# Optimization experiments

Measured on AMD Instinct MI355X. Metric: run time of the kernel, lower is better.

The kernel has to match this reference:

```python
import jax, jax.numpy as jnp
import numpy as np

N_NODES = 100000
N_EDGES = 1600000
D_FEAT = 32
K = 5


def _spmm(edge_row, edge_col, edge_vals, feat):
    # y[i] = sum_{e: row[e]==i} vals[e] * feat[col[e]]  -- sparse A @ feat
    msgs = edge_vals[:, None] * feat[edge_col]  # [E, d]
    return jax.ops.segment_sum(msgs, edge_row, num_segments=N_NODES)


def setup_inputs() -> dict:
    key = jax.random.key(0)
    k1, k2, k3, k4, k5 = jax.random.split(key, 5)
    feat = jax.random.normal(k1, (N_NODES, D_FEAT), dtype=jnp.float32)
    # approximate D^{-1/2} A D^{-1/2} magnitudes: ~1/avg_degree so spectrum stays bounded
    edge_vals = jax.random.uniform(k2, (N_EDGES,), dtype=jnp.float32) * (1.0 / 16.0)
    theta = jnp.asarray([0.5, 0.4, 0.3, 0.2, 0.1], dtype=jnp.float32)
    edge_row = jax.random.randint(k3, (N_EDGES,), 0, N_NODES, dtype=jnp.int32)
    edge_col = jax.random.randint(k4, (N_EDGES,), 0, N_NODES, dtype=jnp.int32)
    return {"feat": feat, "edge_vals": edge_vals, "theta": theta,
            "edge_row": edge_row, "edge_col": edge_col}


def reference(feat, edge_vals, theta, edge_row, edge_col):
    # h = theta[0]*feat; for k>=1: feat = feat - A@feat; h += theta[k]*feat
    h = theta[0] * feat
    for k in range(1, K):
        feat = feat - _spmm(edge_row, edge_col, edge_vals, feat)
        h = h + theta[k] * feat
    return h
```

## Files before the change

kernel.cpp:

```cpp
#include <hip/hip_runtime.h>

#define N_NODES 100000
#define N_EDGES 1600000
#define D_FEAT 32
#define KPOLY 5

#define NWIN 512
#define RPW  ((N_NODES + NWIN - 1) / NWIN)
#define WPAD 16
#define CAP  4096

#define VAL_SCALE 524288.0f
#define VAL_INV   (1.0f / 524288.0f)

#define EB_BS  256
#define EB_EPT 16
#define EB_EPB (EB_BS * EB_EPT)
#define EB_NB  ((N_EDGES + EB_EPB - 1) / EB_EPB)

__device__ __forceinline__ unsigned short f2bf(float f) {
    unsigned u = __float_as_uint(f);
    unsigned r = u + 0x7fffu + ((u >> 16) & 1u);
    return (unsigned short)(r >> 16);
}
__device__ __forceinline__ float bfl(unsigned u) { return __uint_as_float(u << 16); }
__device__ __forceinline__ float bfh(unsigned u) { return __uint_as_float(u & 0xffff0000u); }


__global__ void init_and_bf16_kernel(int* __restrict__ win_cursor,
                                     const float* __restrict__ feat,
                                     unsigned short* __restrict__ out, int n4) {
    int i = blockIdx.x * blockDim.x + threadIdx.x;
    if (i < NWIN) win_cursor[i * WPAD] = i * CAP;
    if (i >= n4) return;
    float4 f = reinterpret_cast<const float4*>(feat)[i];
    ushort4 o;
    o.x = f2bf(f.x); o.y = f2bf(f.y); o.z = f2bf(f.z); o.w = f2bf(f.w);
    reinterpret_cast<ushort4*>(out)[i] = o;
}


__global__ __launch_bounds__(EB_BS) void bucket_kernel(const int* __restrict__ row,
                                                       const int* __restrict__ col,
                                                       const float* __restrict__ vals,
                                                       int* __restrict__ win_cursor,
                                                       uint2* __restrict__ pile) {
    __shared__ int wcnt[NWIN];
    __shared__ int wbase[NWIN];
    int t = threadIdx.x;
    for (int i = t; i < NWIN; i += EB_BS) wcnt[i] = 0;
    __syncthreads();
    int base = blockIdx.x * EB_EPB;
    int w_[EB_EPT];
    int r_[EB_EPT];
#pragma unroll
    for (int i = 0; i < EB_EPT; ++i) {
        int e = base + i * EB_BS + t;
        if (e < N_EDGES) {
            int r = row[e];
            int w = r / RPW;
            r_[i] = r; w_[i] = w;
            atomicAdd(&wcnt[w], 1);
        } else w_[i] = -1;
    }
    __syncthreads();
    for (int i = t; i < NWIN; i += EB_BS) {
        wbase[i] = wcnt[i] ? atomicAdd(&win_cursor[i * WPAD], wcnt[i]) : 0;
        wcnt[i] = 0;
    }
    __syncthreads();
#pragma unroll
    for (int i = 0; i < EB_EPT; ++i) {
        int w = w_[i];
        if (w < 0) continue;
        int e = base + i * EB_BS + t;
        int loc = atomicAdd(&wcnt[w], 1);
        unsigned fx = (unsigned)__float2int_rn(vals[e] * VAL_SCALE);
        if (fx > 0x7FFFu) fx = 0x7FFFu;
        uint2 ed;
        ed.x = ((unsigned)col[e] << 15) | fx;
        ed.y = (unsigned)(r_[i] - w * RPW);
        pile[wbase[w] + loc] = ed;
    }
}

__global__ __launch_bounds__(256) void finesort_kernel(const uint2* __restrict__ pile,
                                                       const int* __restrict__ win_cursor,
                                                       unsigned int* __restrict__ cvout,
                                                       int2* __restrict__ row_rng) {
    __shared__ int cnt[256];
    __shared__ int incl[256];
    __shared__ int cur[256];
    int w = blockIdx.x, t = threadIdx.x;
    int rbeg = w * RPW;
    int rcnt = N_NODES - rbeg;
    if (rcnt > RPW) rcnt = RPW;
    if (rcnt < 0) rcnt = 0;
    int pbeg = w * CAP;
    int pend = win_cursor[w * WPAD];
    cnt[t] = 0;
    __syncthreads();
    for (int i = pbeg + t; i < pend; i += 256) atomicAdd(&cnt[pile[i].y], 1);
    __syncthreads();
    int v = cnt[t];
    incl[t] = v;
    __syncthreads();
    for (int off = 1; off < 256; off <<= 1) {
        int u = (t >= off) ? incl[t - off] : 0;
        __syncthreads();
        incl[t] += u;
        __syncthreads();
    }
    int ex = incl[t] - v;
    if (t < rcnt) {
        cur[t] = ex;
        row_rng[rbeg + t] = make_int2(pbeg + ex, pbeg + ex + v);
    }
    __syncthreads();
    for (int i = pbeg + t; i < pend; i += 256) {
        uint2 ed = pile[i];
        int pos = atomicAdd(&cur[ed.y], 1);
        cvout[pbeg + pos] = ed.x;
    }
}


__global__ __launch_bounds__(256) void spmm_kernel(const int2* __restrict__ row_rng,
                               const unsigned int* __restrict__ cv,
                               const unsigned short* __restrict__ gsrc,
                               const float* __restrict__ feat,
                               unsigned short* __restrict__ g_out,
                               float* __restrict__ h,
                               const float* __restrict__ theta,
                               int k, int first, int write_cur) {
    int tid = blockIdx.x * blockDim.x + threadIdx.x;
    int r = tid >> 2;
    int c = tid & 3;
    if (r >= N_NODES) return;
    float t = theta[k];
    int2 rng = row_rng[r];
    int e = rng.x, end = rng.y;
    float a0=0.f,a1=0.f,a2=0.f,a3=0.f,a4=0.f,a5=0.f,a6=0.f,a7=0.f;

    for (; e + 4 <= end; e += 4) {
        unsigned p0 = cv[e + 0];
        unsigned p1 = cv[e + 1];
        unsigned p2 = cv[e + 2];
        unsigned p3 = cv[e + 3];
        uint4 q0 = *(reinterpret_cast<const uint4*>(gsrc + (size_t)(p0 >> 15) * D_FEAT) + c);
        uint4 q1 = *(reinterpret_cast<const uint4*>(gsrc + (size_t)(p1 >> 15) * D_FEAT) + c);
        uint4 q2 = *(reinterpret_cast<const uint4*>(gsrc + (size_t)(p2 >> 15) * D_FEAT) + c);
        uint4 q3 = *(reinterpret_cast<const uint4*>(gsrc + (size_t)(p3 >> 15) * D_FEAT) + c);
        float v0 = (float)(p0 & 0x7FFFu) * VAL_INV;
        float v1 = (float)(p1 & 0x7FFFu) * VAL_INV;
        float v2 = (float)(p2 & 0x7FFFu) * VAL_INV;
        float v3 = (float)(p3 & 0x7FFFu) * VAL_INV;
        a0 += v0 * bfl(q0.x); a1 += v0 * bfh(q0.x); a2 += v0 * bfl(q0.y); a3 += v0 * bfh(q0.y);
        a4 += v0 * bfl(q0.z); a5 += v0 * bfh(q0.z); a6 += v0 * bfl(q0.w); a7 += v0 * bfh(q0.w);
        a0 += v1 * bfl(q1.x); a1 += v1 * bfh(q1.x); a2 += v1 * bfl(q1.y); a3 += v1 * bfh(q1.y);
        a4 += v1 * bfl(q1.z); a5 += v1 * bfh(q1.z); a6 += v1 * bfl(q1.w); a7 += v1 * bfh(q1.w);
        a0 += v2 * bfl(q2.x); a1 += v2 * bfh(q2.x); a2 += v2 * bfl(q2.y); a3 += v2 * bfh(q2.y);
        a4 += v2 * bfl(q2.z); a5 += v2 * bfh(q2.z); a6 += v2 * bfl(q2.w); a7 += v2 * bfh(q2.w);
        a0 += v3 * bfl(q3.x); a1 += v3 * bfh(q3.x); a2 += v3 * bfl(q3.y); a3 += v3 * bfh(q3.y);
        a4 += v3 * bfl(q3.z); a5 += v3 * bfh(q3.z); a6 += v3 * bfl(q3.w); a7 += v3 * bfh(q3.w);
    }
    for (; e < end; ++e) {
        unsigned p = cv[e];
        float v = (float)(p & 0x7FFFu) * VAL_INV;
        uint4 q = *(reinterpret_cast<const uint4*>(gsrc + (size_t)(p >> 15) * D_FEAT) + c);
        a0 += v * bfl(q.x); a1 += v * bfh(q.x); a2 += v * bfl(q.y); a3 += v * bfh(q.y);
        a4 += v * bfl(q.z); a5 += v * bfh(q.z); a6 += v * bfl(q.w); a7 += v * bfh(q.w);
    }

    size_t base = (size_t)r * D_FEAT + c * 8;
    float c0,c1,c2,c3,c4,c5,c6,c7;
    if (first) {
        float4 f0 = *reinterpret_cast<const float4*>(feat + base);
        float4 f1 = *reinterpret_cast<const float4*>(feat + base + 4);
        c0=f0.x; c1=f0.y; c2=f0.z; c3=f0.w; c4=f1.x; c5=f1.y; c6=f1.z; c7=f1.w;
    } else {
        uint4 q = *reinterpret_cast<const uint4*>(gsrc + base);
        c0=bfl(q.x); c1=bfh(q.x); c2=bfl(q.y); c3=bfh(q.y);
        c4=bfl(q.z); c5=bfh(q.z); c6=bfl(q.w); c7=bfh(q.w);
    }
    float n0=c0-a0, n1=c1-a1, n2=c2-a2, n3=c3-a3, n4=c4-a4, n5=c5-a5, n6=c6-a6, n7=c7-a7;
    if (write_cur) {
        uint4 o;
        o.x = (unsigned)f2bf(n0) | ((unsigned)f2bf(n1) << 16);
        o.y = (unsigned)f2bf(n2) | ((unsigned)f2bf(n3) << 16);
        o.z = (unsigned)f2bf(n4) | ((unsigned)f2bf(n5) << 16);
        o.w = (unsigned)f2bf(n6) | ((unsigned)f2bf(n7) << 16);
        *reinterpret_cast<uint4*>(g_out + base) = o;
    }
    float4 h0, h1;
    if (first) {
        float t0 = theta[0];
        h0.x = t0*c0; h0.y = t0*c1; h0.z = t0*c2; h0.w = t0*c3;
        h1.x = t0*c4; h1.y = t0*c5; h1.z = t0*c6; h1.w = t0*c7;
    } else {
        h0 = *reinterpret_cast<float4*>(h + base);
        h1 = *reinterpret_cast<float4*>(h + base + 4);
    }
    h0.x += t*n0; h0.y += t*n1; h0.z += t*n2; h0.w += t*n3;
    h1.x += t*n4; h1.y += t*n5; h1.z += t*n6; h1.w += t*n7;
    *reinterpret_cast<float4*>(h + base) = h0;
    *reinterpret_cast<float4*>(h + base + 4) = h1;
}

extern "C" void kernel_launch(void* const* d_in, const int* in_sizes, int n_in,
                              void* d_out, int out_size, void* d_ws, size_t ws_size,
                              hipStream_t stream) {
    const float* feat  = (const float*)d_in[0];
    const float* vals  = (const float*)d_in[1];
    const float* theta = (const float*)d_in[2];
    const int*   row   = (const int*)d_in[3];
    const int*   col   = (const int*)d_in[4];
    float* h = (float*)d_out;

    char* ws = (char*)d_ws;
    size_t off = 0;
    auto alloc = [&](size_t bytes) { void* p = ws + off; off = (off + bytes + 63) & ~(size_t)63; return p; };
    unsigned short* feat16 = (unsigned short*)alloc((size_t)N_NODES * D_FEAT * sizeof(short));
    unsigned short* T1 = (unsigned short*)alloc((size_t)N_NODES * D_FEAT * sizeof(short));
    unsigned short* T2 = (unsigned short*)alloc((size_t)N_NODES * D_FEAT * sizeof(short));
    unsigned short* T3 = (unsigned short*)alloc((size_t)N_NODES * D_FEAT * sizeof(short));
    int2*  row_rng  = (int2*)alloc((size_t)N_NODES * sizeof(int2));
    int*   win_cursor = (int*)alloc((size_t)NWIN * WPAD * sizeof(int));
    uint2* pile     = (uint2*)alloc((size_t)NWIN * CAP * sizeof(uint2));
    unsigned int* cv = (unsigned int*)alloc((size_t)NWIN * CAP * sizeof(unsigned int));

    const int blk = 256;
    const int n4 = N_NODES * D_FEAT / 4;

    init_and_bf16_kernel<<<(n4 + blk - 1) / blk, blk, 0, stream>>>(win_cursor, feat, feat16, n4);
    bucket_kernel<<<EB_NB, EB_BS, 0, stream>>>(row, col, vals, win_cursor, pile);
    finesort_kernel<<<NWIN, 256, 0, stream>>>(pile, win_cursor, cv, row_rng);

    const int sgrid = (N_NODES * 4 + blk - 1) / blk;
    spmm_kernel<<<sgrid, blk, 0, stream>>>(row_rng, cv, feat16, feat, T1, h, theta, 1, 1, 1);
    spmm_kernel<<<sgrid, blk, 0, stream>>>(row_rng, cv, T1, feat, T2, h, theta, 2, 0, 1);
    spmm_kernel<<<sgrid, blk, 0, stream>>>(row_rng, cv, T2, feat, T3, h, theta, 3, 0, 1);
    spmm_kernel<<<sgrid, blk, 0, stream>>>(row_rng, cv, T3, feat, T1, h, theta, 4, 0, 0);
}
```

Measured before the change: 151.8 us.

## Stage bucketed edges in shared memory for coalesced scatter to window piles

The bucket kernel now computes a block-local exclusive prefix sum of per-window counts and first writes packed edges into a shared-memory staging buffer sorted by window. A second pass then writes the staged edges to the global pile in contiguous runs per window, replacing scattered per-thread global stores. Edge packing also moves into the first pass so col and vals are read while row is loaded. This adds 32KB of LDS, extra syncs and a scan, which may lower occupancy.

```diff
diff --git a/kernel.cpp b/kernel.cpp
--- a/kernel.cpp
+++ b/kernel.cpp
@@ -46,41 +46,69 @@
                                                        int* __restrict__ win_cursor,
                                                        uint2* __restrict__ pile) {
     __shared__ int wcnt[NWIN];
+    __shared__ int lbase[NWIN];
     __shared__ int wbase[NWIN];
+    __shared__ int ps[EB_BS];
+    __shared__ uint2 stage[EB_EPB];
     int t = threadIdx.x;
     for (int i = t; i < NWIN; i += EB_BS) wcnt[i] = 0;
     __syncthreads();
+
     int base = blockIdx.x * EB_EPB;
-    int w_[EB_EPT];
-    int r_[EB_EPT];
+    unsigned pk_[EB_EPT];
+    int wr_[EB_EPT];
 #pragma unroll
     for (int i = 0; i < EB_EPT; ++i) {
         int e = base + i * EB_BS + t;
         if (e < N_EDGES) {
             int r = row[e];
             int w = r / RPW;
-            r_[i] = r; w_[i] = w;
+            unsigned fx = (unsigned)__float2int_rn(vals[e] * VAL_SCALE);
+            if (fx > 0x7FFFu) fx = 0x7FFFu;
+            pk_[i] = ((unsigned)col[e] << 15) | fx;
+            wr_[i] = (w << 8) | (r - w * RPW);
             atomicAdd(&wcnt[w], 1);
-        } else w_[i] = -1;
-    }
-    __syncthreads();
+        } else wr_[i] = -1;
+    }
+    __syncthreads();
+
+    int c0 = wcnt[2 * t], c1 = wcnt[2 * t + 1];
+    ps[t] = c0 + c1;
+    __syncthreads();
+    for (int off = 1; off < EB_BS; off <<= 1) {
+        int u = (t >= off) ? ps[t - off] : 0;
+        __syncthreads();
+        ps[t] += u;
+        __syncthreads();
+    }
+    int pex = ps[t] - (c0 + c1);
+    lbase[2 * t]     = pex;
+    lbase[2 * t + 1] = pex + c0;
+    __syncthreads();
+
     for (int i = t; i < NWIN; i += EB_BS) {
-        wbase[i] = wcnt[i] ? atomicAdd(&win_cursor[i * WPAD], wcnt[i]) : 0;
-        wcnt[i] = 0;
-    }
-    __syncthreads();
+        int cw = wcnt[i];
+        wbase[i] = cw ? atomicAdd(&win_cursor[i * WPAD], cw) : 0;
+    }
+    __syncthreads();
+    for (int i = t; i < NWIN; i += EB_BS) wcnt[i] = lbase[i];
+    __syncthreads();
+
 #pragma unroll
     for (int i = 0; i < EB_EPT; ++i) {
-        int w = w_[i];
-        if (w < 0) continue;
-        int e = base + i * EB_BS + t;
+        if (wr_[i] < 0) continue;
+        int w = wr_[i] >> 8;
         int loc = atomicAdd(&wcnt[w], 1);
-        unsigned fx = (unsigned)__float2int_rn(vals[e] * VAL_SCALE);
-        if (fx > 0x7FFFu) fx = 0x7FFFu;
-        uint2 ed;
-        ed.x = ((unsigned)col[e] << 15) | fx;
-        ed.y = (unsigned)(r_[i] - w * RPW);
-        pile[wbase[w] + loc] = ed;
+        stage[loc] = make_uint2(pk_[i], (unsigned)wr_[i]);
+    }
+    __syncthreads();
+
+    int nedge = N_EDGES - base; if (nedge > EB_EPB) nedge = EB_EPB;
+    for (int i = t; i < nedge; i += EB_BS) {
+        uint2 ed = stage[i];
+        int w = ed.y >> 8;
+        int pos = wbase[w] + (i - lbase[w]);
+        pile[pos] = make_uint2(ed.x, ed.y & 0xFFu);
     }
 }
 
```

After: 146.8 us. 1.03x faster.
